# Optimization experiments

Hardware: AMD Instinct MI355X
Metric: run time of the kernel (lower is better)

The kernel has to match this reference:

```python
import jax, jax.numpy as jnp
import numpy as np

N = 20000    # num nodes
E = 320000   # num edges (also rows of edge_type, SPN line-graph style)
F = 64       # num_features
HID = 64     # hidden_channels
HEADS = 4    # gatv2_heads
NC = 2       # num_classes
PH = 128     # proxy hidden size
SLOPE = 0.2  # PyG GATv2 leaky_relu negative slope


def gatv2(feat, src, dst, wl, wr, att, b, num_nodes, concat):
    # GATv2Conv (PyG semantics, add_self_loops=True, dropout off in eval)
    H, C = att.shape
    xl = (feat @ wl).reshape(-1, H, C)
    xr = (feat @ wr).reshape(-1, H, C)
    loops = jnp.arange(num_nodes, dtype=src.dtype)
    s = jnp.concatenate([src, loops])
    d = jnp.concatenate([dst, loops])
    e = jax.nn.leaky_relu(xl[s] + xr[d], SLOPE)            # [E', H, C]
    logits = jnp.einsum('ehc,hc->eh', e, att)              # [E', H]
    m = jax.ops.segment_max(logits, d, num_segments=num_nodes)
    p = jnp.exp(logits - m[d])
    z = jax.ops.segment_sum(p, d, num_segments=num_nodes)
    alpha = p / z[d]                                       # segment softmax
    out = jax.ops.segment_sum(xl[s] * alpha[:, :, None], d, num_segments=num_nodes)
    out = out.reshape(num_nodes, H * C) if concat else out.mean(axis=1)
    return out + b


def setup_inputs():
    key = jax.random.key(0)
    ks = iter(jax.random.split(key, 32))
    def rn(shape, scale=0.1):
        return jax.random.normal(next(ks), shape, dtype=jnp.float32) * scale
    return {
        'x': rn((N, F), 1.0),
        'edge_type': rn((E, F), 1.0),
        'edge_index': jax.random.randint(next(ks), (2, E), 0, N, dtype=jnp.int32),
        'n1_wl': rn((F, HEADS * HID)), 'n1_wr': rn((F, HEADS * HID)),
        'n1_att': rn((HEADS, HID)), 'n1_b': jnp.zeros((HEADS * HID,), jnp.float32),
        'n2_wl': rn((HEADS * HID, HID)), 'n2_wr': rn((HEADS * HID, HID)),
        'n2_att': rn((1, HID)), 'n2_b': jnp.zeros((HID,), jnp.float32),
        'e1_wl': rn((F, HEADS * HID)), 'e1_wr': rn((F, HEADS * HID)),
        'e1_att': rn((HEADS, HID)), 'e1_b': jnp.zeros((HEADS * HID,), jnp.float32),
        'e2_wl': rn((HEADS * HID, HID)), 'e2_wr': rn((HEADS * HID, HID)),
        'e2_att': rn((1, HID)), 'e2_b': jnp.zeros((HID,), jnp.float32),
        'crf_wu': rn((HID, NC)), 'crf_bu': jnp.zeros((NC,), jnp.float32),
        'crf_wp': rn((HID, NC)),
        'px_w1': rn((HID, PH)), 'px_b1': jnp.zeros((PH,), jnp.float32),
        'px_w2': rn((PH, NC)), 'px_b2': jnp.zeros((NC,), jnp.float32),
    }


def reference(x, edge_type, edge_index, n1_wl, n1_wr, n1_att, n1_b, n2_wl, n2_wr, n2_att, n2_b,
              e1_wl, e1_wr, e1_att, e1_b, e2_wl, e2_wr, e2_att, e2_b,
              crf_wu, crf_bu, crf_wp, px_w1, px_b1, px_w2, px_b2):
    src, dst = edge_index[0], edge_index[1]
    # node GNN: GATv2 -> ELU -> GATv2 (dropout = identity in eval)
    h = jax.nn.elu(gatv2(x, src, dst, n1_wl, n1_wr, n1_att, n1_b, N, True))
    node_repr = gatv2(h, src, dst, n2_wl, n2_wr, n2_att, n2_b, N, False)
    # edge GNN over edge features (E rows, same edge_index, per source code)
    g = jax.nn.elu(gatv2(edge_type, src, dst, e1_wl, e1_wr, e1_att, e1_b, E, True))
    edge_repr = gatv2(g, src, dst, e2_wl, e2_wr, e2_att, e2_b, E, False)
    # CRF head: unary potentials + pairwise messages scattered to dst nodes
    unary = node_repr @ crf_wu + crf_bu
    msg = jax.ops.segment_sum(edge_repr @ crf_wp, dst, num_segments=N)
    crf_out = jax.nn.log_softmax(unary + msg, axis=-1)
    # MLP proxy head
    ph = jax.nn.relu(node_repr @ px_w1 + px_b1)
    proxy_out = ph @ px_w2 + px_b2
    return crf_out, proxy_out
```

## Files before the change

kernel.cpp:

```cpp
#include <hip/hip_runtime.h>
#include <cstddef>
#include <cstdint>

#define N_NODES 20000
#define N_EDGES 320000

typedef __attribute__((ext_vector_type(8))) short bf8_t;
typedef __attribute__((ext_vector_type(4))) float f4_t;
typedef __attribute__((ext_vector_type(2))) float f2_t;
typedef unsigned short bfu;
typedef __attribute__((ext_vector_type(4))) unsigned short us4_t;
typedef __attribute__((ext_vector_type(8))) unsigned short us8_t;

__device__ __forceinline__ short f2bf(float f) {
  unsigned u = __float_as_uint(f);
  u += 0x7fff + ((u >> 16) & 1);
  return (short)(u >> 16);
}
__device__ __forceinline__ f2_t leaky2(f2_t t) {
  f2_t zero = {0.f, 0.f};
  f2_t mx = __builtin_elementwise_max(t, zero);
  f2_t mn = __builtin_elementwise_min(t, zero);
  return mn * 0.2f + mx;
}
__device__ __forceinline__ void bf8_to_f2x4(us8_t xu, f2_t o[4]) {
  union { us8_t v; unsigned u[4]; } c; c.v = xu;
  #pragma unroll
  for (int j = 0; j < 4; ++j) {
    unsigned d = c.u[j];
    f2_t t;
    t.x = __uint_as_float(d << 16);
    t.y = __uint_as_float(d & 0xffff0000u);
    o[j] = t;
  }
}

__global__ void count_deg_kernel(const int* __restrict__ dst, int* __restrict__ deg, int e_cnt) {
  int e = blockIdx.x * blockDim.x + threadIdx.x;
  if (e < e_cnt) atomicAdd(&deg[dst[e]], 1);
}

__global__ __launch_bounds__(1024) void scan_kernel(
    const int* __restrict__ deg, int* __restrict__ rowptr,
    int* __restrict__ cursor, int n) {
  __shared__ int sdata[1024];
  const int CH = (n + 1023) / 1024;
  int tid = threadIdx.x;
  int base = tid * CH;
  int loc[20];
  int s = 0;
  for (int j = 0; j < CH; ++j) {
    int idx = base + j;
    int v = (idx < n) ? deg[idx] : 0;
    loc[j] = s;
    s += v;
  }
  sdata[tid] = s;
  __syncthreads();
  for (int off = 1; off < 1024; off <<= 1) {
    int t = (tid >= off) ? sdata[tid - off] : 0;
    __syncthreads();
    sdata[tid] += t;
    __syncthreads();
  }
  int excl = sdata[tid] - s;
  for (int j = 0; j < CH; ++j) {
    int idx = base + j;
    if (idx < n) { int val = excl + loc[j]; rowptr[idx] = val; cursor[idx] = val; }
  }
  if (tid == 0) rowptr[n] = sdata[1023];
}

__global__ void fill_csr_kernel(const int* __restrict__ src, const int* __restrict__ dst,
                                int* __restrict__ cursor, int* __restrict__ csr_src,
                                int* __restrict__ csr_eid, int e_cnt) {
  int e = blockIdx.x * blockDim.x + threadIdx.x;
  if (e < e_cnt) {
    int pos = atomicAdd(&cursor[dst[e]], 1);
    csr_src[pos] = src[e];
    csr_eid[pos] = e;
  }
}

__global__ void prep_all_kernel(
    const float* __restrict__ n1l, const float* __restrict__ n1r,
    const float* __restrict__ e1l, const float* __restrict__ e1r,
    const float* __restrict__ n2l, const float* __restrict__ n2r,
    const float* __restrict__ e2l, const float* __restrict__ e2r,
    const float* __restrict__ b2, const float* __restrict__ wp,
    short* __restrict__ t_n1l, short* __restrict__ t_n1r,
    short* __restrict__ t_e1l, short* __restrict__ t_e1r,
    short* __restrict__ t_n2l, short* __restrict__ t_n2r,
    short* __restrict__ t_e2l, short* __restrict__ t_e2r,
    float* __restrict__ wct, float* __restrict__ pc)
{
  int i = blockIdx.x * blockDim.x + threadIdx.x;
  int seg = i >> 14;
  int j = i & 16383;
  if (seg < 4) {
    const float* srcs[4] = {n1l, n1r, e1l, e1r};
    short* dsts[4] = {t_n1l, t_n1r, t_e1l, t_e1r};
    int n = j >> 6, k = j & 63;
    dsts[seg][n * 64 + k] = f2bf(srcs[seg][k * 256 + n]);
  } else if (seg < 8) {
    const float* srcs[4] = {n2l, n2r, e2l, e2r};
    short* dsts[4] = {t_n2l, t_n2r, t_e2l, t_e2r};
    int n = j >> 8, k = j & 255;
    dsts[seg - 4][n * 256 + k] = f2bf(srcs[seg - 4][k * 64 + n]);
  } else if (seg == 8) {
    if (j < 512) {
      int jj = j & 1;
      int k  = j >> 1;
      float s = 0.f;
      for (int c = 0; c < 64; ++c) s = fmaf(e2l[k * 64 + c], wp[c * 2 + jj], s);
      wct[jj * 256 + k] = s;
    } else if (j < 514) {
      int jj = j - 512;
      float s = 0.f;
      for (int c = 0; c < 64; ++c) s = fmaf(b2[c], wp[c * 2 + jj], s);
      pc[jj] = s;
    }
  }
}

template<int K>
__global__ __launch_bounds__(128) void mfma_proj2_kernel(
    const float* __restrict__ A0,
    const short* __restrict__ Wtl0, const short* __restrict__ Wtr0,
    bfu* __restrict__ xl0, float* __restrict__ xr0,
    const float* __restrict__ A1,
    const short* __restrict__ Wtl1, const short* __restrict__ Wtr1,
    bfu* __restrict__ xl1, float* __restrict__ xr1,
    int M, int nslices)
{
  constexpr int KC = K / 32;
  int tid = threadIdx.x;
  int w = tid >> 6, lane = tid & 63, quad = lane >> 4, l15 = lane & 15;
  int row_base = (int)blockIdx.x * 64 + w * 32;
  int y = (int)blockIdx.y;
  int z = (int)blockIdx.z;
  const float* A = z ? A1 : A0;
  bool is_l = y < nslices;
  const short* Wt = z ? (is_l ? Wtl1 : Wtr1) : (is_l ? Wtl0 : Wtr0);
  bfu* xl = z ? xl1 : xl0;
  float* xr = z ? xr1 : xr0;
  int cb = (is_l ? y : y - nslices) * 64;
  int STR = nslices * 64;

  bf8_t a[2][KC];
  #pragma unroll
  for (int rt = 0; rt < 2; ++rt) {
    int r = row_base + rt * 16 + l15;
    int rc = r < M ? r : M - 1;
    const float* ap = A + (size_t)rc * K + quad * 8;
    #pragma unroll
    for (int kc = 0; kc < KC; ++kc) {
      float4 v0 = *(const float4*)(ap + kc * 32);
      float4 v1 = *(const float4*)(ap + kc * 32 + 4);
      bf8_t f;
      f[0] = f2bf(v0.x); f[1] = f2bf(v0.y); f[2] = f2bf(v0.z); f[3] = f2bf(v0.w);
      f[4] = f2bf(v1.x); f[5] = f2bf(v1.y); f[6] = f2bf(v1.z); f[7] = f2bf(v1.w);
      a[rt][kc] = f;
    }
  }

  #pragma unroll
  for (int nt = 0; nt < 4; ++nt) {
    f4_t acc0 = {0.f, 0.f, 0.f, 0.f};
    f4_t acc1 = {0.f, 0.f, 0.f, 0.f};
    const short* wb = Wt + (size_t)(cb + nt * 16 + l15) * K + quad * 8;
    #pragma unroll
    for (int kc = 0; kc < KC; ++kc) {
      bf8_t wf = *(const bf8_t*)(wb + kc * 32);
      acc0 = __builtin_amdgcn_mfma_f32_16x16x32_bf16(wf, a[0][kc], acc0, 0, 0, 0);
      acc1 = __builtin_amdgcn_mfma_f32_16x16x32_bf16(wf, a[1][kc], acc1, 0, 0, 0);
    }
    #pragma unroll
    for (int rt = 0; rt < 2; ++rt) {
      f4_t acc = rt == 0 ? acc0 : acc1;
      int row = row_base + rt * 16 + l15;
      if (row >= M) continue;
      int col = cb + nt * 16 + quad * 4;
      if (is_l) {
        us4_t pk;
        pk[0] = (bfu)f2bf(acc[0]); pk[1] = (bfu)f2bf(acc[1]);
        pk[2] = (bfu)f2bf(acc[2]); pk[3] = (bfu)f2bf(acc[3]);
        *(us4_t*)&xl[(size_t)row * STR + col] = pk;
      } else {
        *(float4*)&xr[(size_t)row * STR + col] = make_float4(acc[0], acc[1], acc[2], acc[3]);
      }
    }
  }
}

template<int KIN>
__device__ __forceinline__ void gemm_body(
    const float* __restrict__ A, const float* __restrict__ W, int wld, int cb,
    int block_m, int M, float (&acc)[8][4],
    float (*As)[128 + 4], float (*Ws)[64 + 4])
{
  int tid = threadIdx.x;
  int tx = tid & 15;
  int ty = tid >> 4;
  #pragma unroll
  for (int i = 0; i < 8; ++i)
    #pragma unroll
    for (int j = 0; j < 4; ++j) acc[i][j] = 0.f;

  for (int k0 = 0; k0 < KIN; k0 += 16) {
    #pragma unroll
    for (int rep = 0; rep < 2; ++rep) {
      int ar = (tid >> 2) + rep * 64;
      int ak = (tid & 3) * 4;
      int gr = block_m + ar;
      float4 v = make_float4(0.f, 0.f, 0.f, 0.f);
      if (gr < M) v = *(const float4*)&A[(size_t)gr * KIN + k0 + ak];
      As[ak + 0][ar] = v.x; As[ak + 1][ar] = v.y;
      As[ak + 2][ar] = v.z; As[ak + 3][ar] = v.w;
    }
    {
      int wr = tid >> 4;
      int wc = (tid & 15) * 4;
      float4 v = *(const float4*)&W[(size_t)(k0 + wr) * wld + cb + wc];
      Ws[wr][wc + 0] = v.x; Ws[wr][wc + 1] = v.y;
      Ws[wr][wc + 2] = v.z; Ws[wr][wc + 3] = v.w;
    }
    __syncthreads();
    #pragma unroll
    for (int k = 0; k < 16; ++k) {
      float a[8], w[4];
      #pragma unroll
      for (int i = 0; i < 8; ++i) a[i] = As[k][ty * 8 + i];
      #pragma unroll
      for (int j = 0; j < 4; ++j) w[j] = Ws[k][tx * 4 + j];
      #pragma unroll
      for (int i = 0; i < 8; ++i)
        #pragma unroll
        for (int j = 0; j < 4; ++j) acc[i][j] = fmaf(a[i], w[j], acc[i][j]);
    }
    __syncthreads();
  }
}

template<int KIN, int MODE>
__global__ __launch_bounds__(256) void gemm64_kernel(
    const float* __restrict__ A, const float* __restrict__ W, int wld,
    const float* __restrict__ bias, float* __restrict__ out, int old, int M)
{
  __shared__ float As[16][128 + 4];
  __shared__ float Ws[16][64 + 4];
  float acc[8][4];
  int block_m = (int)blockIdx.x * 128;
  int cb = (int)blockIdx.y * 64;
  gemm_body<KIN>(A, W, wld, cb, block_m, M, acc, As, Ws);

  int tid = threadIdx.x;
  int tx = tid & 15, ty = tid >> 4;
  int gc = cb + tx * 4;
  #pragma unroll
  for (int i = 0; i < 8; ++i) {
    int gr = block_m + ty * 8 + i;
    if (gr >= M) continue;
    size_t idx = (size_t)gr * old + gc;
    float t0 = acc[i][0], t1 = acc[i][1], t2 = acc[i][2], t3 = acc[i][3];
    if (MODE == 3) {
      t0 = fmaxf(t0 + bias[gc + 0], 0.f);
      t1 = fmaxf(t1 + bias[gc + 1], 0.f);
      t2 = fmaxf(t2 + bias[gc + 2], 0.f);
      t3 = fmaxf(t3 + bias[gc + 3], 0.f);
    }
    *(float4*)&out[idx] = make_float4(t0, t1, t2, t3);
  }
}

template<int STR, bool ELU, bool FUSEP>
__global__ __launch_bounds__(256) void gat_agg_v5(
    const bfu* __restrict__ xl0, const float* __restrict__ xr0,
    const float* __restrict__ att0, const float* __restrict__ bias0,
    float* __restrict__ out0,
    const bfu* __restrict__ xl1, const float* __restrict__ xr1,
    const float* __restrict__ att1, const float* __restrict__ bias1,
    float* __restrict__ out1,
    const int* __restrict__ rowptr, const int* __restrict__ csr_src,
    const float* __restrict__ wp, float* __restrict__ pbuf)
{
  constexpr int HEADS = STR / 64;
  constexpr int GRP = N_NODES / 4;
  int tid = threadIdx.x;
  int w = tid >> 6;
  int lane = tid & 63;
  int egrp = lane >> 3;
  int cch  = lane & 7;

  int bid = (int)blockIdx.x;
  int per_chain = HEADS * GRP;
  int chain = bid >= per_chain ? 1 : 0;
  int r = bid - chain * per_chain;
  int head = r / GRP;
  int d = (r - head * GRP) * 4 + w;

  const bfu* xl = chain ? xl1 : xl0;
  const float* xr = chain ? xr1 : xr0;
  const float* att = chain ? att1 : att0;
  const float* bias = chain ? bias1 : bias0;

  int row0 = rowptr[d];
  int deg = rowptr[d + 1] - row0;
  int cbase = head * 64 + cch * 8;

  f2_t xr2[4], att2[4];
  {
    const float* xrp = xr + (size_t)d * STR + cbase;
    const float* atp = att + cbase;
    float4 a0 = *(const float4*)(xrp);
    float4 a1 = *(const float4*)(xrp + 4);
    xr2[0] = f2_t{a0.x, a0.y}; xr2[1] = f2_t{a0.z, a0.w};
    xr2[2] = f2_t{a1.x, a1.y}; xr2[3] = f2_t{a1.z, a1.w};
    float4 b0 = *(const float4*)(atp);
    float4 b1 = *(const float4*)(atp + 4);
    att2[0] = f2_t{b0.x, b0.y}; att2[1] = f2_t{b0.z, b0.w};
    att2[2] = f2_t{b1.x, b1.y}; att2[3] = f2_t{b1.z, b1.w};
  }

  auto ld_idx = [&](int k) -> int {
    int idx = k * 8 + egrp;
    int cl = idx < deg ? idx : (deg > 0 ? deg - 1 : 0);
    int pos = deg > 0 ? row0 + cl : 0;
    int sv = csr_src[pos];
    return idx < deg ? sv : d;
  };

  float zloc;
  f2_t acc4[4];
  {
    us8_t xu = *(const us8_t*)&xl[(size_t)d * STR + cbase];
    f2_t xs[4];
    bf8_to_f2x4(xu, xs);
    f2_t p2 = {0.f, 0.f};
    #pragma unroll
    for (int j = 0; j < 4; ++j) p2 = p2 + leaky2(xs[j] + xr2[j]) * att2[j];
    float part = p2.x + p2.y;
    part += __shfl_xor(part, 1, 64);
    part += __shfl_xor(part, 2, 64);
    part += __shfl_xor(part, 4, 64);
    float wgt = __expf(part);
    float ws = (egrp == 0) ? wgt : 0.f;
    zloc = ws;
    f2_t ws2 = {ws, ws};
    #pragma unroll
    for (int j = 0; j < 4; ++j) acc4[j] = xs[j] * ws2;
  }

  int C = (deg + 7) >> 3;
  int s_cur = ld_idx(0);
  us8_t xu_cur = *(const us8_t*)&xl[(size_t)s_cur * STR + cbase];
  int s_nxt = ld_idx(1);
  for (int k = 0; k < C; ++k) {
    us8_t xu_nxt = *(const us8_t*)&xl[(size_t)s_nxt * STR + cbase];
    int s_n2 = ld_idx(k + 2);
    bool valid = (k * 8 + egrp) < deg;
    f2_t xf[4];
    bf8_to_f2x4(xu_cur, xf);
    f2_t p2 = {0.f, 0.f};
    #pragma unroll
    for (int i = 0; i < 4; ++i) p2 = p2 + leaky2(xf[i] + xr2[i]) * att2[i];
    float part = p2.x + p2.y;
    part += __shfl_xor(part, 1, 64);
    part += __shfl_xor(part, 2, 64);
    part += __shfl_xor(part, 4, 64);
    float wgt = valid ? __expf(part) : 0.f;
    zloc += wgt;
    f2_t w2 = {wgt, wgt};
    #pragma unroll
    for (int i = 0; i < 4; ++i) acc4[i] = acc4[i] + xf[i] * w2;
    xu_cur = xu_nxt;
    s_nxt = s_n2;
  }

  float a8[8];
  #pragma unroll
  for (int i = 0; i < 4; ++i) { a8[2 * i] = acc4[i].x; a8[2 * i + 1] = acc4[i].y; }
  #pragma unroll
  for (int off = 8; off < 64; off <<= 1) {
    zloc += __shfl_xor(zloc, off, 64);
    #pragma unroll
    for (int i = 0; i < 8; ++i) a8[i] += __shfl_xor(a8[i], off, 64);
  }

  float invz = 1.f / zloc;
  float o[8];
  #pragma unroll
  for (int i = 0; i < 8; ++i) {
    float val = a8[i] * invz + bias[cbase + i];
    if (ELU) val = val > 0.f ? val : __expf(val) - 1.f;
    o[i] = val;
  }

  if (FUSEP && chain) {
    float p0 = 0.f, p1 = 0.f;
    #pragma unroll
    for (int i = 0; i < 8; ++i) {
      float2 wv = *(const float2*)&wp[(cbase + i) * 2];
      p0 = fmaf(o[i], wv.x, p0);
      p1 = fmaf(o[i], wv.y, p1);
    }
    p0 += __shfl_xor(p0, 1, 64); p1 += __shfl_xor(p1, 1, 64);
    p0 += __shfl_xor(p0, 2, 64); p1 += __shfl_xor(p1, 2, 64);
    p0 += __shfl_xor(p0, 4, 64); p1 += __shfl_xor(p1, 4, 64);
    if (lane == 0) *(float2*)&pbuf[2 * d] = make_float2(p0, p1);
  } else if (egrp == 0) {
    float* out = chain ? out1 : out0;
    float* op = out + (size_t)d * STR + cbase;
    *(float4*)(op)     = make_float4(o[0], o[1], o[2], o[3]);
    *(float4*)(op + 4) = make_float4(o[4], o[5], o[6], o[7]);
  }
}

__global__ __launch_bounds__(256) void chunk_fold_kernel(
    const float* __restrict__ A,
    const short* __restrict__ W1t,
    const float* __restrict__ b1,
    const float* __restrict__ WcT,
    const float* __restrict__ pc,
    float* __restrict__ pbufN,
    int Mtot)
{
  int tid = threadIdx.x;
  int w = tid >> 6;
  int lane = tid & 63;
  int quad = lane >> 4;
  int l15 = lane & 15;
  int row_base = (int)blockIdx.x * 256 + w * 64;

  bf8_t a1[4][2];
  #pragma unroll
  for (int rt = 0; rt < 4; ++rt) {
    int r = row_base + rt * 16 + l15;
    int rc = r < Mtot ? r : Mtot - 1;
    const float* ap = A + (size_t)rc * 64 + quad * 8;
    #pragma unroll
    for (int ks = 0; ks < 2; ++ks) {
      float4 v0 = *(const float4*)(ap + ks * 32);
      float4 v1 = *(const float4*)(ap + ks * 32 + 4);
      bf8_t f;
      f[0] = f2bf(v0.x); f[1] = f2bf(v0.y); f[2] = f2bf(v0.z); f[3] = f2bf(v0.w);
      f[4] = f2bf(v1.x); f[5] = f2bf(v1.y); f[6] = f2bf(v1.z); f[7] = f2bf(v1.w);
      a1[rt][ks] = f;
    }
  }

  float p0[4] = {0.f, 0.f, 0.f, 0.f};
  float p1[4] = {0.f, 0.f, 0.f, 0.f};

  #pragma unroll
  for (int cc = 0; cc < 4; ++cc) {
    #pragma unroll
    for (int nt = 0; nt < 4; ++nt) {
      const short* wb = W1t + (cc * 64 + nt * 16 + l15) * 64 + quad * 8;
      bf8_t w0 = *(const bf8_t*)(wb);
      bf8_t w1 = *(const bf8_t*)(wb + 32);
      f4_t g[4];
      #pragma unroll
      for (int rt = 0; rt < 4; ++rt) {
        f4_t z = {0.f, 0.f, 0.f, 0.f};
        z = __builtin_amdgcn_mfma_f32_16x16x32_bf16(w0, a1[rt][0], z, 0, 0, 0);
        z = __builtin_amdgcn_mfma_f32_16x16x32_bf16(w1, a1[rt][1], z, 0, 0, 0);
        g[rt] = z;
      }
      int cbase = cc * 64 + nt * 16 + quad * 4;
      f4_t b4  = *(const f4_t*)&b1[cbase];
      f4_t wc0 = *(const f4_t*)&WcT[cbase];
      f4_t wc1 = *(const f4_t*)&WcT[256 + cbase];
      #pragma unroll
      for (int rt = 0; rt < 4; ++rt) {
        #pragma unroll
        for (int r = 0; r < 4; ++r) {
          float v = g[rt][r] + b4[r];
          v = v > 0.f ? v : __expf(v) - 1.f;
          p0[rt] = fmaf(v, wc0[r], p0[rt]);
          p1[rt] = fmaf(v, wc1[r], p1[rt]);
        }
      }
    }
  }

  #pragma unroll
  for (int off = 16; off < 64; off <<= 1) {
    #pragma unroll
    for (int rt = 0; rt < 4; ++rt) {
      p0[rt] += __shfl_xor(p0[rt], off, 64);
      p1[rt] += __shfl_xor(p1[rt], off, 64);
    }
  }
  if (quad == 0) {
    float c0 = pc[0], c1 = pc[1];
    #pragma unroll
    for (int rt = 0; rt < 4; ++rt) {
      int row = row_base + rt * 16 + l15;
      if (row < Mtot)
        *(float2*)&pbufN[2 * row] = make_float2(p0[rt] + c0, p1[rt] + c1);
    }
  }
}

__global__ void head_kernel(const float* __restrict__ node_repr, const float* __restrict__ ph,
                            const int* __restrict__ rowptr, const int* __restrict__ csr_eid,
                            const float* __restrict__ pbuf, const float* __restrict__ wu,
                            const float* __restrict__ bu, const float* __restrict__ w2,
                            const float* __restrict__ b2, float* __restrict__ out, int n) {
  __shared__ float swu[128];
  __shared__ float sw2[256];
  int tid = threadIdx.x;
  if (tid < 128) swu[tid] = wu[tid];
  sw2[tid] = w2[tid];
  __syncthreads();
  int i = blockIdx.x * blockDim.x + tid;
  if (i >= n) return;
  float m0 = 0.f, m1 = 0.f;
  int r0 = rowptr[i], r1 = rowptr[i + 1];
  int jj = r0;
  for (; jj + 4 <= r1; jj += 4) {
    int e0 = csr_eid[jj + 0], e1 = csr_eid[jj + 1];
    int e2 = csr_eid[jj + 2], e3 = csr_eid[jj + 3];
    float2 q0 = *(const float2*)&pbuf[2 * e0];
    float2 q1 = *(const float2*)&pbuf[2 * e1];
    float2 q2 = *(const float2*)&pbuf[2 * e2];
    float2 q3 = *(const float2*)&pbuf[2 * e3];
    m0 += (q0.x + q1.x) + (q2.x + q3.x);
    m1 += (q0.y + q1.y) + (q2.y + q3.y);
  }
  for (; jj < r1; ++jj) {
    int e = csr_eid[jj];
    float2 q = *(const float2*)&pbuf[2 * e];
    m0 += q.x; m1 += q.y;
  }
  const float* nr = node_repr + (size_t)i * 64;
  float u0 = bu[0], u1 = bu[1];
  #pragma unroll
  for (int k = 0; k < 64; ++k) {
    float v = nr[k];
    u0 = fmaf(v, swu[2 * k + 0], u0);
    u1 = fmaf(v, swu[2 * k + 1], u1);
  }
  float v0 = u0 + m0;
  float v1 = u1 + m1;
  float mx = fmaxf(v0, v1);
  float lse = mx + logf(__expf(v0 - mx) + __expf(v1 - mx));
  out[2 * i + 0] = v0 - lse;
  out[2 * i + 1] = v1 - lse;
  const float* p = ph + (size_t)i * 128;
  float p0 = b2[0], p1 = b2[1];
  #pragma unroll
  for (int k = 0; k < 128; ++k) {
    float v = p[k];
    p0 = fmaf(v, sw2[2 * k + 0], p0);
    p1 = fmaf(v, sw2[2 * k + 1], p1);
  }
  out[2 * n + 2 * i + 0] = p0;
  out[2 * n + 2 * i + 1] = p1;
}

extern "C" void kernel_launch(void* const* d_in, const int* in_sizes, int n_in,
                              void* d_out, int out_size, void* d_ws, size_t ws_size,
                              hipStream_t stream) {
  const int N = N_NODES, E = N_EDGES;
  const float* x         = (const float*)d_in[0];
  const float* edge_type = (const float*)d_in[1];
  const int*   ei        = (const int*)d_in[2];
  const float* n1_wl  = (const float*)d_in[3];
  const float* n1_wr  = (const float*)d_in[4];
  const float* n1_att = (const float*)d_in[5];
  const float* n1_b   = (const float*)d_in[6];
  const float* n2_wl  = (const float*)d_in[7];
  const float* n2_wr  = (const float*)d_in[8];
  const float* n2_att = (const float*)d_in[9];
  const float* n2_b   = (const float*)d_in[10];
  const float* e1_wl  = (const float*)d_in[11];
  const float* e1_wr  = (const float*)d_in[12];
  const float* e1_att = (const float*)d_in[13];
  const float* e1_b   = (const float*)d_in[14];
  const float* e2_wl  = (const float*)d_in[15];
  const float* e2_wr  = (const float*)d_in[16];
  const float* e2_att = (const float*)d_in[17];
  const float* e2_b   = (const float*)d_in[18];
  const float* crf_wu = (const float*)d_in[19];
  const float* crf_bu = (const float*)d_in[20];
  const float* crf_wp = (const float*)d_in[21];
  const float* px_w1  = (const float*)d_in[22];
  const float* px_b1  = (const float*)d_in[23];
  const float* px_w2  = (const float*)d_in[24];
  const float* px_b2  = (const float*)d_in[25];
  float* out = (float*)d_out;
  const int* src = ei;
  const int* dst = ei + E;
  (void)in_sizes; (void)n_in; (void)out_size; (void)ws_size;

  char* ws = (char*)d_ws;
  size_t off = 0;
  auto alloc = [&](size_t bytes) -> void* {
    void* p = ws + off;
    off += (bytes + 255) & ~(size_t)255;
    return p;
  };
  bfu*   xl_n  = (bfu*)alloc((size_t)N * 256 * 2);
  float* xr_n  = (float*)alloc((size_t)N * 256 * 4);
  bfu*   xl_e  = (bfu*)alloc((size_t)N * 256 * 2);
  float* xr_e  = (float*)alloc((size_t)N * 256 * 4);
  float* h_n   = (float*)alloc((size_t)N * 256 * 4);
  float* g_e   = (float*)alloc((size_t)N * 256 * 4);
  bfu*   xl2_n = (bfu*)alloc((size_t)N * 64 * 2);
  float* xr2_n = (float*)alloc((size_t)N * 64 * 4);
  bfu*   xl2_e = (bfu*)alloc((size_t)N * 64 * 2);
  float* xr2_e = (float*)alloc((size_t)N * 64 * 4);
  float* B3    = (float*)alloc((size_t)N * 64 * 4);
  float* pbuf  = (float*)alloc((size_t)E * 2 * 4);
  float* ph    = (float*)(void*)xl_n;
  int* deg     = (int*)alloc((size_t)N * 4);
  int* rowptr  = (int*)alloc((size_t)(N + 1) * 4);
  int* cursor  = (int*)alloc((size_t)N * 4);
  int* csr_src = (int*)alloc((size_t)E * 4);
  int* csr_eid = (int*)alloc((size_t)E * 4);
  short* t_n1l = (short*)alloc((size_t)16384 * 2);
  short* t_n1r = (short*)alloc((size_t)16384 * 2);
  short* t_e1l = (short*)alloc((size_t)16384 * 2);
  short* t_e1r = (short*)alloc((size_t)16384 * 2);
  short* t_n2l = (short*)alloc((size_t)16384 * 2);
  short* t_n2r = (short*)alloc((size_t)16384 * 2);
  short* t_e2l = (short*)alloc((size_t)16384 * 2);
  short* t_e2r = (short*)alloc((size_t)16384 * 2);
  float* WcT   = (float*)alloc((size_t)2 * 256 * 4);
  float* pcv   = (float*)alloc((size_t)2 * 4);

  const int EB = (E + 255) / 256;
  const int NB = (N + 127) / 128;
  const int PB = (N + 63) / 64;
  const int Mhigh = E - N;
  const int CFB = (Mhigh + 255) / 256;
  const int GRP = N / 4;

  hipMemsetAsync(deg, 0, (size_t)N * 4, stream);
  count_deg_kernel<<<EB, 256, 0, stream>>>(dst, deg, E);
  scan_kernel<<<1, 1024, 0, stream>>>(deg, rowptr, cursor, N);
  fill_csr_kernel<<<EB, 256, 0, stream>>>(src, dst, cursor, csr_src, csr_eid, E);
  prep_all_kernel<<<515, 256, 0, stream>>>(n1_wl, n1_wr, e1_wl, e1_wr,
                                           n2_wl, n2_wr, e2_wl, e2_wr,
                                           e2_b, crf_wp,
                                           t_n1l, t_n1r, t_e1l, t_e1r,
                                           t_n2l, t_n2r, t_e2l, t_e2r, WcT, pcv);

  mfma_proj2_kernel<64><<<dim3(PB, 8, 2), 128, 0, stream>>>(
      x, t_n1l, t_n1r, xl_n, xr_n,
      edge_type, t_e1l, t_e1r, xl_e, xr_e, N, 4);
  gat_agg_v5<256, true, false><<<2 * 4 * GRP, 256, 0, stream>>>(
      xl_n, xr_n, n1_att, n1_b, h_n,
      xl_e, xr_e, e1_att, e1_b, g_e, rowptr, csr_src, nullptr, nullptr);

  mfma_proj2_kernel<256><<<dim3(PB, 2, 2), 128, 0, stream>>>(
      h_n, t_n2l, t_n2r, xl2_n, xr2_n,
      g_e, t_e2l, t_e2r, xl2_e, xr2_e, N, 1);
  gat_agg_v5<64, false, true><<<2 * GRP, 256, 0, stream>>>(
      xl2_n, xr2_n, n2_att, n2_b, B3,
      xl2_e, xr2_e, e2_att, e2_b, nullptr, rowptr, csr_src, crf_wp, pbuf);

  chunk_fold_kernel<<<CFB, 256, 0, stream>>>(edge_type + (size_t)N * 64, t_e1l,
                                             e1_b, WcT, pcv, pbuf + 2 * (size_t)N, Mhigh);

  gemm64_kernel<64, 3><<<dim3(NB, 2), 256, 0, stream>>>(B3, px_w1, 128, px_b1, ph, 128, N);
  head_kernel<<<(N + 255) / 256, 256, 0, stream>>>(B3, ph, rowptr, csr_eid, pbuf,
                                                   crf_wu, crf_bu, px_w2, px_b2, out, N);
}
```

Baseline: 459.9 us.

## Store projections in fp16 and compute attention logits with packed half math

Switches the xl/xr projection outputs from bf16/fp32 to fp16, which halves xr storage and gather traffic. The attention logit (add, leaky relu, dot with att) now runs in packed half2 arithmetic using fdot2 with fp32 accumulation. Index math moves to 32-bit unsigned, and chunk_fold is relaunched with 64-thread blocks instead of 256. The risks are reduced accuracy and possible fp16 overflow in the leaky-relu intermediate values.

Result: no change. 456.6 us (-0.7%).

```diff
diff --git a/kernel.cpp b/kernel.cpp
--- a/kernel.cpp
+++ b/kernel.cpp
@@ -9,30 +9,29 @@
 typedef __attribute__((ext_vector_type(4))) float f4_t;
 typedef __attribute__((ext_vector_type(2))) float f2_t;
 typedef unsigned short bfu;
-typedef __attribute__((ext_vector_type(4))) unsigned short us4_t;
-typedef __attribute__((ext_vector_type(8))) unsigned short us8_t;
+typedef _Float16 half_t;
+typedef __attribute__((ext_vector_type(2))) _Float16 h2_t;
+typedef __attribute__((ext_vector_type(4))) _Float16 h4_t;
+typedef __attribute__((ext_vector_type(8))) _Float16 h8_t;
 
 __device__ __forceinline__ short f2bf(float f) {
   unsigned u = __float_as_uint(f);
   u += 0x7fff + ((u >> 16) & 1);
   return (short)(u >> 16);
 }
-__device__ __forceinline__ f2_t leaky2(f2_t t) {
-  f2_t zero = {0.f, 0.f};
-  f2_t mx = __builtin_elementwise_max(t, zero);
-  f2_t mn = __builtin_elementwise_min(t, zero);
-  return mn * 0.2f + mx;
-}
-__device__ __forceinline__ void bf8_to_f2x4(us8_t xu, f2_t o[4]) {
-  union { us8_t v; unsigned u[4]; } c; c.v = xu;
-  #pragma unroll
-  for (int j = 0; j < 4; ++j) {
-    unsigned d = c.u[j];
-    f2_t t;
-    t.x = __uint_as_float(d << 16);
-    t.y = __uint_as_float(d & 0xffff0000u);
-    o[j] = t;
-  }
+__device__ __forceinline__ h2_t leaky_h2(h2_t t) {
+  h2_t zero = {(_Float16)0.f, (_Float16)0.f};
+  h2_t mx = __builtin_elementwise_max(t, zero);
+  h2_t mn = __builtin_elementwise_min(t, zero);
+  h2_t c  = {(_Float16)0.2f, (_Float16)0.2f};
+  return mn * c + mx;
+}
+__device__ __forceinline__ float dot2h(h2_t a, h2_t b, float c) {
+#if __has_builtin(__builtin_amdgcn_fdot2)
+  return __builtin_amdgcn_fdot2(a, b, c, false);
+#else
+  return c + (float)a.x * (float)b.x + (float)a.y * (float)b.y;
+#endif
 }
 
 __global__ void count_deg_kernel(const int* __restrict__ dst, int* __restrict__ deg, int e_cnt) {
@@ -127,10 +126,10 @@
 __global__ __launch_bounds__(128) void mfma_proj2_kernel(
     const float* __restrict__ A0,
     const short* __restrict__ Wtl0, const short* __restrict__ Wtr0,
-    bfu* __restrict__ xl0, float* __restrict__ xr0,
+    half_t* __restrict__ xl0, half_t* __restrict__ xr0,
     const float* __restrict__ A1,
     const short* __restrict__ Wtl1, const short* __restrict__ Wtr1,
-    bfu* __restrict__ xl1, float* __restrict__ xr1,
+    half_t* __restrict__ xl1, half_t* __restrict__ xr1,
     int M, int nslices)
 {
   constexpr int KC = K / 32;
@@ -142,8 +141,7 @@
   const float* A = z ? A1 : A0;
   bool is_l = y < nslices;
   const short* Wt = z ? (is_l ? Wtl1 : Wtr1) : (is_l ? Wtl0 : Wtr0);
-  bfu* xl = z ? xl1 : xl0;
-  float* xr = z ? xr1 : xr0;
+  half_t* dst = z ? (is_l ? xl1 : xr1) : (is_l ? xl0 : xr0);
   int cb = (is_l ? y : y - nslices) * 64;
   int STR = nslices * 64;
 
@@ -181,14 +179,10 @@
       int row = row_base + rt * 16 + l15;
       if (row >= M) continue;
       int col = cb + nt * 16 + quad * 4;
-      if (is_l) {
-        us4_t pk;
-        pk[0] = (bfu)f2bf(acc[0]); pk[1] = (bfu)f2bf(acc[1]);
-        pk[2] = (bfu)f2bf(acc[2]); pk[3] = (bfu)f2bf(acc[3]);
-        *(us4_t*)&xl[(size_t)row * STR + col] = pk;
-      } else {
-        *(float4*)&xr[(size_t)row * STR + col] = make_float4(acc[0], acc[1], acc[2], acc[3]);
-      }
+      h4_t pk;
+      pk[0] = (_Float16)acc[0]; pk[1] = (_Float16)acc[1];
+      pk[2] = (_Float16)acc[2]; pk[3] = (_Float16)acc[3];
+      *(h4_t*)&dst[(size_t)row * STR + col] = pk;
     }
   }
 }
@@ -274,11 +268,11 @@
 }
 
 template<int STR, bool ELU, bool FUSEP>
-__global__ __launch_bounds__(256) void gat_agg_v5(
-    const bfu* __restrict__ xl0, const float* __restrict__ xr0,
+__global__ __launch_bounds__(256) void gat_agg_v6(
+    const half_t* __restrict__ xl0, const half_t* __restrict__ xr0,
     const float* __restrict__ att0, const float* __restrict__ bias0,
     float* __restrict__ out0,
-    const bfu* __restrict__ xl1, const float* __restrict__ xr1,
+    const half_t* __restrict__ xl1, const half_t* __restrict__ xr1,
     const float* __restrict__ att1, const float* __restrict__ bias1,
     float* __restrict__ out1,
     const int* __restrict__ rowptr, const int* __restrict__ csr_src,
@@ -299,8 +293,8 @@
   int head = r / GRP;
   int d = (r - head * GRP) * 4 + w;
 
-  const bfu* xl = chain ? xl1 : xl0;
-  const float* xr = chain ? xr1 : xr0;
+  const half_t* xl = chain ? xl1 : xl0;
+  const half_t* xr = chain ? xr1 : xr0;
   const float* att = chain ? att1 : att0;
   const float* bias = chain ? bias1 : bias0;
 
@@ -308,18 +302,18 @@
   int deg = rowptr[d + 1] - row0;
   int cbase = head * 64 + cch * 8;
 
-  f2_t xr2[4], att2[4];
+  h2_t xr2[4], att2[4];
   {
-    const float* xrp = xr + (size_t)d * STR + cbase;
+    h8_t xv = *(const h8_t*)&xr[(unsigned)(d * STR + cbase)];
+    xr2[0] = h2_t{xv[0], xv[1]}; xr2[1] = h2_t{xv[2], xv[3]};
+    xr2[2] = h2_t{xv[4], xv[5]}; xr2[3] = h2_t{xv[6], xv[7]};
     const float* atp = att + cbase;
-    float4 a0 = *(const float4*)(xrp);
-    float4 a1 = *(const float4*)(xrp + 4);
-    xr2[0] = f2_t{a0.x, a0.y}; xr2[1] = f2_t{a0.z, a0.w};
-    xr2[2] = f2_t{a1.x, a1.y}; xr2[3] = f2_t{a1.z, a1.w};
     float4 b0 = *(const float4*)(atp);
     float4 b1 = *(const float4*)(atp + 4);
-    att2[0] = f2_t{b0.x, b0.y}; att2[1] = f2_t{b0.z, b0.w};
-    att2[2] = f2_t{b1.x, b1.y}; att2[3] = f2_t{b1.z, b1.w};
+    att2[0] = h2_t{(_Float16)b0.x, (_Float16)b0.y};
+    att2[1] = h2_t{(_Float16)b0.z, (_Float16)b0.w};
+    att2[2] = h2_t{(_Float16)b1.x, (_Float16)b1.y};
+    att2[3] = h2_t{(_Float16)b1.z, (_Float16)b1.w};
   }
 
   auto ld_idx = [&](int k) -> int {
@@ -333,46 +327,52 @@
   float zloc;
   f2_t acc4[4];
   {
-    us8_t xu = *(const us8_t*)&xl[(size_t)d * STR + cbase];
-    f2_t xs[4];
-    bf8_to_f2x4(xu, xs);
-    f2_t p2 = {0.f, 0.f};
-    #pragma unroll
-    for (int j = 0; j < 4; ++j) p2 = p2 + leaky2(xs[j] + xr2[j]) * att2[j];
-    float part = p2.x + p2.y;
+    h8_t xu = *(const h8_t*)&xl[(unsigned)(d * STR + cbase)];
+    h2_t xs[4];
+    xs[0] = h2_t{xu[0], xu[1]}; xs[1] = h2_t{xu[2], xu[3]};
+    xs[2] = h2_t{xu[4], xu[5]}; xs[3] = h2_t{xu[6], xu[7]};
+    float part = 0.f;
+    #pragma unroll
+    for (int j = 0; j < 4; ++j) part = dot2h(leaky_h2(xs[j] + xr2[j]), att2[j], part);
     part += __shfl_xor(part, 1, 64);
     part += __shfl_xor(part, 2, 64);
     part += __shfl_xor(part, 4, 64);
     float wgt = __expf(part);
     float ws = (egrp == 0) ? wgt : 0.f;
     zloc = ws;
-    f2_t ws2 = {ws, ws};
-    #pragma unroll
-    for (int j = 0; j < 4; ++j) acc4[j] = xs[j] * ws2;
+    #pragma unroll
+    for (int j = 0; j < 4; ++j) {
+      f2_t t;
+      t.x = (float)xs[j].x * ws;
+      t.y = (float)xs[j].y * ws;
+      acc4[j] = t;
+    }
   }
 
   int C = (deg + 7) >> 3;
   int s_cur = ld_idx(0);
-  us8_t xu_cur = *(const us8_t*)&xl[(size_t)s_cur * STR + cbase];
+  h8_t xu_cur = *(const h8_t*)&xl[(unsigned)(s_cur * STR + cbase)];
   int s_nxt = ld_idx(1);
   for (int k = 0; k < C; ++k) {
-    us8_t xu_nxt = *(const us8_t*)&xl[(size_t)s_nxt * STR + cbase];
+    h8_t xu_nxt = *(const h8_t*)&xl[(unsigned)(s_nxt * STR + cbase)];
     int s_n2 = ld_idx(k + 2);
     bool valid = (k * 8 + egrp) < deg;
-    f2_t xf[4];
-    bf8_to_f2x4(xu_cur, xf);
-    f2_t p2 = {0.f, 0.f};
-    #pragma unroll
-    for (int i = 0; i < 4; ++i) p2 = p2 + leaky2(xf[i] + xr2[i]) * att2[i];
-    float part = p2.x + p2.y;
+    h2_t xf[4];
+    xf[0] = h2_t{xu_cur[0], xu_cur[1]}; xf[1] = h2_t{xu_cur[2], xu_cur[3]};
+    xf[2] = h2_t{xu_cur[4], xu_cur[5]}; xf[3] = h2_t{xu_cur[6], xu_cur[7]};
+    float part = 0.f;
+    #pragma unroll
+    for (int i = 0; i < 4; ++i) part = dot2h(leaky_h2(xf[i] + xr2[i]), att2[i], part);
     part += __shfl_xor(part, 1, 64);
     part += __shfl_xor(part, 2, 64);
     part += __shfl_xor(part, 4, 64);
     float wgt = valid ? __expf(part) : 0.f;
     zloc += wgt;
-    f2_t w2 = {wgt, wgt};
-    #pragma unroll
-    for (int i = 0; i < 4; ++i) acc4[i] = acc4[i] + xf[i] * w2;
+    #pragma unroll
+    for (int i = 0; i < 4; ++i) {
+      acc4[i].x = fmaf((float)xf[i].x, wgt, acc4[i].x);
+      acc4[i].y = fmaf((float)xf[i].y, wgt, acc4[i].y);
+    }
     xu_cur = xu_nxt;
     s_nxt = s_n2;
   }
@@ -416,7 +416,7 @@
   }
 }
 
-__global__ __launch_bounds__(256) void chunk_fold_kernel(
+__global__ __launch_bounds__(64) void chunk_fold_kernel(
     const float* __restrict__ A,
     const short* __restrict__ W1t,
     const float* __restrict__ b1,
@@ -425,12 +425,10 @@
     float* __restrict__ pbufN,
     int Mtot)
 {
-  int tid = threadIdx.x;
-  int w = tid >> 6;
-  int lane = tid & 63;
+  int lane = threadIdx.x;
   int quad = lane >> 4;
   int l15 = lane & 15;
-  int row_base = (int)blockIdx.x * 256 + w * 64;
+  int row_base = (int)blockIdx.x * 64;
 
   bf8_t a1[4][2];
   #pragma unroll
@@ -602,16 +600,16 @@
     off += (bytes + 255) & ~(size_t)255;
     return p;
   };
-  bfu*   xl_n  = (bfu*)alloc((size_t)N * 256 * 2);
-  float* xr_n  = (float*)alloc((size_t)N * 256 * 4);
-  bfu*   xl_e  = (bfu*)alloc((size_t)N * 256 * 2);
-  float* xr_e  = (float*)alloc((size_t)N * 256 * 4);
+  half_t* xl_n  = (half_t*)alloc((size_t)N * 256 * 2);
+  half_t* xr_n  = (half_t*)alloc((size_t)N * 256 * 2);
+  half_t* xl_e  = (half_t*)alloc((size_t)N * 256 * 2);
+  half_t* xr_e  = (half_t*)alloc((size_t)N * 256 * 2);
   float* h_n   = (float*)alloc((size_t)N * 256 * 4);
   float* g_e   = (float*)alloc((size_t)N * 256 * 4);
-  bfu*   xl2_n = (bfu*)alloc((size_t)N * 64 * 2);
-  float* xr2_n = (float*)alloc((size_t)N * 64 * 4);
-  bfu*   xl2_e = (bfu*)alloc((size_t)N * 64 * 2);
-  float* xr2_e = (float*)alloc((size_t)N * 64 * 4);
+  half_t* xl2_n = (half_t*)alloc((size_t)N * 64 * 2);
+  half_t* xr2_n = (half_t*)alloc((size_t)N * 64 * 2);
+  half_t* xl2_e = (half_t*)alloc((size_t)N * 64 * 2);
+  half_t* xr2_e = (half_t*)alloc((size_t)N * 64 * 2);
   float* B3    = (float*)alloc((size_t)N * 64 * 4);
   float* pbuf  = (float*)alloc((size_t)E * 2 * 4);
   float* ph    = (float*)(void*)xl_n;
@@ -635,7 +633,7 @@
   const int NB = (N + 127) / 128;
   const int PB = (N + 63) / 64;
   const int Mhigh = E - N;
-  const int CFB = (Mhigh + 255) / 256;
+  const int CFB = (Mhigh + 63) / 64;
   const int GRP = N / 4;
 
   hipMemsetAsync(deg, 0, (size_t)N * 4, stream);
@@ -651,19 +649,19 @@
   mfma_proj2_kernel<64><<<dim3(PB, 8, 2), 128, 0, stream>>>(
       x, t_n1l, t_n1r, xl_n, xr_n,
       edge_type, t_e1l, t_e1r, xl_e, xr_e, N, 4);
-  gat_agg_v5<256, true, false><<<2 * 4 * GRP, 256, 0, stream>>>(
+  gat_agg_v6<256, true, false><<<2 * 4 * GRP, 256, 0, stream>>>(
       xl_n, xr_n, n1_att, n1_b, h_n,
       xl_e, xr_e, e1_att, e1_b, g_e, rowptr, csr_src, nullptr, nullptr);
 
   mfma_proj2_kernel<256><<<dim3(PB, 2, 2), 128, 0, stream>>>(
       h_n, t_n2l, t_n2r, xl2_n, xr2_n,
       g_e, t_e2l, t_e2r, xl2_e, xr2_e, N, 1);
-  gat_agg_v5<64, false, true><<<2 * GRP, 256, 0, stream>>>(
+  gat_agg_v6<64, false, true><<<2 * GRP, 256, 0, stream>>>(
       xl2_n, xr2_n, n2_att, n2_b, B3,
       xl2_e, xr2_e, e2_att, e2_b, nullptr, rowptr, csr_src, crf_wp, pbuf);
 
-  chunk_fold_kernel<<<CFB, 256, 0, stream>>>(edge_type + (size_t)N * 64, t_e1l,
-                                             e1_b, WcT, pcv, pbuf + 2 * (size_t)N, Mhigh);
+  chunk_fold_kernel<<<CFB, 64, 0, stream>>>(edge_type + (size_t)N * 64, t_e1l,
+                                            e1_b, WcT, pcv, pbuf + 2 * (size_t)N, Mhigh);
 
   gemm64_kernel<64, 3><<<dim3(NB, 2), 256, 0, stream>>>(B3, px_w1, 128, px_b1, ph, 128, N);
   head_kernel<<<(N + 255) / 256, 256, 0, stream>>>(B3, ph, rowptr, csr_eid, pbuf,
```
